# Optimization experiments

Measured on AMD Instinct MI355X. Metric: run time of the kernel, lower is better.

## Reference

```python
import jax, jax.numpy as jnp
import numpy as np


def _cumsum_reset_on_zeros(x):
    # Segmented cumsum along the last axis that resets to 0 at positions where x == 0.
    # Equivalent to the torch trick (inject -diff at zero positions then cumsum):
    # result[i] = cumsum(x)[i] - cumsum(x)[last zero position <= i] (0 if none).
    accum = jnp.cumsum(x, axis=-1)
    pos = jnp.arange(x.shape[-1])
    last_zero = jax.lax.cummax(jnp.where(x == 0, pos, -1), axis=x.ndim - 1)
    baseline = jnp.where(last_zero >= 0, accum[jnp.maximum(last_zero, 0)], jnp.zeros((), accum.dtype))
    return accum - baseline


def _shift_right(x):
    # shift last axis right by one, inserting a leading zero (pad+roll+narrow in torch)
    return jnp.concatenate([jnp.zeros((1,), x.dtype), x[:-1]], axis=-1)


def _adsr(gate, attack, decay, sustain, release):
    one = jnp.float32(1.0)
    ad_axis = _cumsum_reset_on_zeros(gate)          # samples since note-on, 0 while gate off
    attack_mask = (ad_axis <= attack).astype(gate.dtype) * gate
    decay_mask = (ad_axis > attack).astype(gate.dtype) * gate
    release_mask = one - gate
    decay_tc = jnp.exp(-one / decay)                # 1/e**(1/decay)
    release_tc = jnp.exp(-one / release)
    decay_slope = sustain + (one - sustain) * jnp.power(decay_tc, ad_axis - attack)

    # ---- release slope: exp of segmented cumsum of log(release_tc), seeded by decay value at note-off
    ri = decay_slope * jnp.roll(release_mask, -1, axis=-1) * decay_mask  # decay value at last gated sample
    ri = _shift_right(ri)                                                # move seed into first release sample
    ri = jnp.where(ri == 0, one, ri)
    ri = ri * (jnp.cumsum(gate, axis=-1) > 0).astype(gate.dtype)         # zero before the first note
    ri = ri * release_mask * release_tc
    log_rs = jnp.where(ri > 0, jnp.log(jnp.where(ri > 0, ri, one)), 0.0)  # log(0) -> 0, as in torch
    cum_log = _cumsum_reset_on_zeros(log_rs)
    release_slope = jnp.where(cum_log == 0, 0.0, jnp.exp(cum_log))        # 0 -> -inf -> exp -> 0

    # ---- attack slope: ramp from the release level at (re)trigger up to 1
    attack_start = release_slope * jnp.roll(attack_mask, -1, axis=-1) * release_mask
    attack_start = jnp.cumsum(_shift_right(attack_start), axis=-1)
    attack_slope = (one - attack_start) * ad_axis / attack + attack_start

    return attack_slope * attack_mask + decay_slope * decay_mask + release_slope * release_mask


def setup_inputs() -> dict:
    T = 1 << 23  # ~175 s of audio at 48 kHz
    phase = jnp.arange(T) % 48000
    # realistic note pattern: gate high for 24000 samples (0.5 s) per 1 s period,
    # starting with a silent region to exercise the pre-first-note path
    gate = ((phase >= 12000) & (phase < 36000)).astype(jnp.float32)
    return {
        "gate": gate,
        "attack": jnp.float32(480.0),
        "decay": jnp.float32(4800.0),
        "sustain": jnp.float32(0.5),
        "release": jnp.float32(9600.0),
    }


def reference(gate, attack, decay, sustain, release):
    return _adsr(gate, attack, decay, sustain, release)
```

## Files before the change

kernel.cpp:

```cpp
#include <hip/hip_runtime.h>
#include <math.h>

#define SEG_CAP 2048
#define SORT_CAP 8192

struct SegRec { float p0; int type; };

__device__ __forceinline__ float wave_scan_f(float v) {
#pragma unroll
    for (int d = 1; d < 64; d <<= 1) {
        float n = __shfl_up(v, d, 64);
        if ((threadIdx.x & 63) >= d) v += n;
    }
    return v;
}

__global__ void k_collect(const float* __restrict__ g, int T,
                          int* __restrict__ trans, int* __restrict__ counter, int cap) {
    const int tid = threadIdx.x;
    const long nq = (long)T >> 2;
    const long stride = (long)gridDim.x * blockDim.x;
    for (long q = (long)blockIdx.x * blockDim.x + tid; q < nq; q += stride) {
        const long i = q << 2;
        const float4 v = *reinterpret_cast<const float4*>(g + i);
        float prev = __shfl_up(v.w, 1, 64);
        if ((tid & 63) == 0) prev = (i > 0) ? g[i - 1] : v.x;
        int m = 0;
        if (v.x != prev) m |= 1;
        if (v.y != v.x)  m |= 2;
        if (v.z != v.y)  m |= 4;
        if (v.w != v.z)  m |= 8;
        if (m) {
            const int c = __popc(m);
            int base = atomicAdd(counter, c);
            if (m & 1) { if (base < cap) trans[base] = (int)i;     ++base; }
            if (m & 2) { if (base < cap) trans[base] = (int)i + 1; ++base; }
            if (m & 4) { if (base < cap) trans[base] = (int)i + 2; ++base; }
            if (m & 8) { if (base < cap) trans[base] = (int)i + 3; ++base; }
        }
    }
    if (blockIdx.x == 0 && tid == 0) {
        for (long i = nq << 2; i < T; ++i) {
            if (i > 0 && g[i] != g[i - 1]) {
                int base = atomicAdd(counter, 1);
                if (base < cap) trans[base] = (int)i;
            }
        }
    }
}

__global__ void __launch_bounds__(1024) k_segs(
    const float* __restrict__ g,
    const int* __restrict__ trans, const int* __restrict__ counter,
    int* __restrict__ seg_starts, SegRec* __restrict__ recs, int* __restrict__ nseg_p,
    const float* __restrict__ attack_p, const float* __restrict__ decay_p,
    const float* __restrict__ sustain_p, const float* __restrict__ release_p) {
    __shared__ int s_tr[SORT_CAP];
    __shared__ float lds[16];
    const int tid = threadIdx.x;
    const int lane = tid & 63, w = tid >> 6;

    int ntrans = *counter;
    if (ntrans > SORT_CAP) ntrans = SORT_CAP;

    int S = 2;
    while (S < ntrans) S <<= 1;
    for (int i = tid; i < S; i += 1024) s_tr[i] = (i < ntrans) ? trans[i] : 0x7FFFFFFF;
    __syncthreads();
    for (int k = 2; k <= S; k <<= 1) {
        for (int jj = k >> 1; jj > 0; jj >>= 1) {
            for (int idx = tid; idx < S; idx += 1024) {
                const int ixj = idx ^ jj;
                if (ixj > idx) {
                    const int a = s_tr[idx], b = s_tr[ixj];
                    const bool up = ((idx & k) == 0);
                    if ((a > b) == up) { s_tr[idx] = b; s_tr[ixj] = a; }
                }
            }
            __syncthreads();
        }
    }

    const float attack = *attack_p, decay = *decay_p;
    const float sustain = *sustain_p, release = *release_p;
    const float dlog2 = log2f(expf(-1.0f / decay));
    const float rlog2 = log2f(expf(-1.0f / release));
    const bool g0 = (g[0] != 0.0f);
    const int nseg = ntrans + 1;
    if (tid == 0) *nseg_p = nseg;

    float carry = 0.0f;
    for (int basej = 0; basej < nseg; basej += 1024) {
        const int j = basej + tid;
        const bool valid = (j < nseg);
        int start = 0;
        bool gated = false;
        float r = 0.0f;
        if (valid) {
            start = (j == 0) ? 0 : s_tr[j - 1];
            gated = ((j & 1) == 0) ? g0 : !g0;
            if (gated && j >= 2) {
                const int startm1 = s_tr[j - 2];
                const int startm2 = (j == 2) ? 0 : s_tr[j - 3];
                const float lenprev = (float)(startm1 - startm2);
                const float seedp = (lenprev > attack)
                                        ? (sustain + (1.0f - sustain) * exp2f((lenprev - attack) * dlog2))
                                        : 1.0f;
                const float gap = (float)(start - startm1);
                if (1.0f <= attack) r = seedp * exp2f(gap * rlog2);
            }
        }
        float s = wave_scan_f(r);
        if (lane == 63) lds[w] = s;
        __syncthreads();
        if (w == 0) {
            float t = (lane < 16) ? lds[lane] : 0.0f;
#pragma unroll
            for (int d = 1; d < 16; d <<= 1) {
                float nn = __shfl_up(t, d, 64);
                if (lane >= d) t += nn;
            }
            if (lane < 16) lds[lane] = t;
        }
        __syncthreads();
        const float add = (w == 0) ? 0.0f : lds[w - 1];
        const float incl = s + add;
        const float tile_total = lds[15];
        if (valid) {
            seg_starts[j] = start;
            SegRec rec;
            if (gated) {
                rec.type = 1;
                rec.p0 = carry + incl;
            } else if (j == 0) {
                rec.type = 0;
                rec.p0 = 0.0f;
            } else {
                const int sp = (j == 1) ? 0 : s_tr[j - 2];
                const float len = (float)(start - sp);
                rec.type = 2;
                rec.p0 = (len > attack)
                             ? (sustain + (1.0f - sustain) * exp2f((len - attack) * dlog2))
                             : 1.0f;
            }
            recs[j] = rec;
        }
        __syncthreads();
        carry += tile_total;
    }
}

__global__ void k_out(float* __restrict__ out, int T,
                      const int* __restrict__ seg_starts, const SegRec* __restrict__ recs,
                      const int* __restrict__ nseg_p,
                      const float* __restrict__ attack_p, const float* __restrict__ decay_p,
                      const float* __restrict__ sustain_p, const float* __restrict__ release_p) {
    __shared__ int s_start[SEG_CAP];
    __shared__ float s_p0[SEG_CAP];
    __shared__ int s_type[SEG_CAP];
    const int nseg = *nseg_p;
    const bool useLds = (nseg <= SEG_CAP);
    if (useLds) {
        for (int j = threadIdx.x; j < nseg; j += blockDim.x) {
            s_start[j] = seg_starts[j];
            SegRec r = recs[j];
            s_p0[j] = r.p0;
            s_type[j] = r.type;
        }
        __syncthreads();
    }
    const float attack = *attack_p, decay = *decay_p;
    const float sustain = *sustain_p, release = *release_p;
    const float dlog2 = log2f(expf(-1.0f / decay));
    const float rlog2 = log2f(expf(-1.0f / release));
    const float inv_attack = 1.0f / attack;

    const long i0 = ((long)blockIdx.x * blockDim.x + threadIdx.x) * 4;
    if (i0 >= T) return;

    int lo = 0, hi = nseg - 1;
    if (useLds) {
        while (lo < hi) { int mid = (lo + hi + 1) >> 1; if (s_start[mid] <= i0) lo = mid; else hi = mid - 1; }
    } else {
        while (lo < hi) { int mid = (lo + hi + 1) >> 1; if (seg_starts[mid] <= i0) lo = mid; else hi = mid - 1; }
    }
    int j = lo;
    float res[4];
#pragma unroll
    for (int e = 0; e < 4; ++e) {
        const long i = i0 + e;
        if (i < T) {
            if (useLds) { while (j + 1 < nseg && s_start[j + 1] <= i) ++j; }
            else        { while (j + 1 < nseg && seg_starts[j + 1] <= i) ++j; }
            const int   type = useLds ? s_type[j] : recs[j].type;
            const float p0   = useLds ? s_p0[j]   : recs[j].p0;
            const int   st   = useLds ? s_start[j] : seg_starts[j];
            float v;
            if (type == 1) {
                const float ad = (float)(i - st + 1);
                if (ad <= attack) v = (1.0f - p0) * ad * inv_attack + p0;
                else              v = sustain + (1.0f - sustain) * exp2f((ad - attack) * dlog2);
            } else if (type == 2) {
                const float k = (float)(i - st + 1);
                v = p0 * exp2f(k * rlog2);
            } else {
                v = 0.0f;
            }
            res[e] = v;
        } else {
            res[e] = 0.0f;
        }
    }
    if (i0 + 3 < T) {
        *reinterpret_cast<float4*>(out + i0) = make_float4(res[0], res[1], res[2], res[3]);
    } else {
        for (int e = 0; e < 4; ++e)
            if (i0 + e < T) out[i0 + e] = res[e];
    }
}

extern "C" void kernel_launch(void* const* d_in, const int* in_sizes, int n_in,
                              void* d_out, int out_size, void* d_ws, size_t ws_size,
                              hipStream_t stream) {
    const float* gate    = (const float*)d_in[0];
    const float* attack  = (const float*)d_in[1];
    const float* decay   = (const float*)d_in[2];
    const float* sustain = (const float*)d_in[3];
    const float* release = (const float*)d_in[4];
    float* out = (float*)d_out;
    const int T = in_sizes[0];

    char* w = (char*)d_ws;
    int* counter = (int*)w;
    int* nseg_p  = (int*)(w + 8);
    int* trans      = (int*)(w + 256);
    int* seg_starts = trans + SORT_CAP;
    SegRec* recs    = (SegRec*)(seg_starts + SORT_CAP + 2);

    hipMemsetAsync(counter, 0, sizeof(int), stream);

    const int collect_blocks = 2048;
    k_collect<<<collect_blocks, 256, 0, stream>>>(gate, T, trans, counter, SORT_CAP);
    k_segs<<<1, 1024, 0, stream>>>(gate, trans, counter, seg_starts, recs, nseg_p,
                                   attack, decay, sustain, release);
    const int g3 = (int)(((long)T / 4 + 255) / 256);
    k_out<<<g3, 256, 0, stream>>>(out, T, seg_starts, recs, nseg_p,
                                  attack, decay, sustain, release);
}
```

Baseline: 56.50 us.

## Replace atomic transition gather and bitonic sort with per-chunk ordered slots and scan

The transition collector now gives each 4096-sample chunk a fixed slot region. Positions are written in order using a block-level prefix scan over per-thread counts, which replaces the global atomic counter. The single-block segment kernel then compacts these slots with a scan, so the bitonic sort and the memset launch are no longer needed. In exchange, any chunk with more than 16 transitions is silently truncated, and the segment kernel now has to loop over all chunk counts (about 2048) serially in one block.

```diff
diff --git a/kernel.cpp b/kernel.cpp
--- a/kernel.cpp
+++ b/kernel.cpp
@@ -1,11 +1,23 @@
 #include <hip/hip_runtime.h>
 #include <math.h>
 
+#define CHUNK 4096
+#define K1_BLOCK 256
+#define EPT 16
+#define KSLOT 16
+#define SORT_CAP 8192
 #define SEG_CAP 2048
-#define SORT_CAP 8192
 
 struct SegRec { float p0; int type; };
 
+__device__ __forceinline__ int wave_scan_i(int v) {
+#pragma unroll
+    for (int d = 1; d < 64; d <<= 1) {
+        int n = __shfl_up(v, d, 64);
+        if ((threadIdx.x & 63) >= d) v += n;
+    }
+    return v;
+}
 __device__ __forceinline__ float wave_scan_f(float v) {
 #pragma unroll
     for (int d = 1; d < 64; d <<= 1) {
@@ -16,70 +28,103 @@
 }
 
 __global__ void k_collect(const float* __restrict__ g, int T,
-                          int* __restrict__ trans, int* __restrict__ counter, int cap) {
+                          int* __restrict__ counts, int* __restrict__ chunk_tr) {
     const int tid = threadIdx.x;
-    const long nq = (long)T >> 2;
-    const long stride = (long)gridDim.x * blockDim.x;
-    for (long q = (long)blockIdx.x * blockDim.x + tid; q < nq; q += stride) {
-        const long i = q << 2;
-        const float4 v = *reinterpret_cast<const float4*>(g + i);
-        float prev = __shfl_up(v.w, 1, 64);
-        if ((tid & 63) == 0) prev = (i > 0) ? g[i - 1] : v.x;
-        int m = 0;
-        if (v.x != prev) m |= 1;
-        if (v.y != v.x)  m |= 2;
-        if (v.z != v.y)  m |= 4;
-        if (v.w != v.z)  m |= 8;
-        if (m) {
-            const int c = __popc(m);
-            int base = atomicAdd(counter, c);
-            if (m & 1) { if (base < cap) trans[base] = (int)i;     ++base; }
-            if (m & 2) { if (base < cap) trans[base] = (int)i + 1; ++base; }
-            if (m & 4) { if (base < cap) trans[base] = (int)i + 2; ++base; }
-            if (m & 8) { if (base < cap) trans[base] = (int)i + 3; ++base; }
-        }
-    }
-    if (blockIdx.x == 0 && tid == 0) {
-        for (long i = nq << 2; i < T; ++i) {
-            if (i > 0 && g[i] != g[i - 1]) {
-                int base = atomicAdd(counter, 1);
-                if (base < cap) trans[base] = (int)i;
-            }
+    const long base = (long)blockIdx.x * CHUNK + (long)tid * EPT;
+    float vals[EPT];
+    float prevFirst = 0.0f;
+    int n = 0;
+    if (base < T) {
+        const long rem = (long)T - base;
+        n = (int)(rem < EPT ? rem : (long)EPT);
+        prevFirst = (base > 0) ? g[base - 1] : 0.0f;
+        if (n == EPT) {
+#pragma unroll
+            for (int q = 0; q < EPT / 4; ++q) {
+                const float4 v = *reinterpret_cast<const float4*>(g + base + q * 4);
+                vals[q * 4 + 0] = v.x; vals[q * 4 + 1] = v.y;
+                vals[q * 4 + 2] = v.z; vals[q * 4 + 3] = v.w;
+            }
+        } else {
+            for (int e = 0; e < n; ++e) vals[e] = g[base + e];
+        }
+    }
+    int c = 0;
+    {
+        float prev = prevFirst;
+        for (int e = 0; e < n; ++e) {
+            const long i = base + e;
+            if (i > 0 && vals[e] != prev) ++c;
+            prev = vals[e];
+        }
+    }
+    __shared__ int lds[K1_BLOCK / 64];
+    const int lane = tid & 63, w = tid >> 6;
+    const int s = wave_scan_i(c);
+    if (lane == 63) lds[w] = s;
+    __syncthreads();
+    int add = 0;
+#pragma unroll
+    for (int q = 0; q < K1_BLOCK / 64; ++q) add += (q < w) ? lds[q] : 0;
+    int pos = s + add - c;
+    const int total = lds[0] + lds[1] + lds[2] + lds[3];
+    if (tid == 0) counts[blockIdx.x] = (total < KSLOT) ? total : KSLOT;
+    {
+        float prev = prevFirst;
+        for (int e = 0; e < n; ++e) {
+            const long i = base + e;
+            if (i > 0 && vals[e] != prev) {
+                if (pos < KSLOT) chunk_tr[(long)blockIdx.x * KSLOT + pos] = (int)i;
+                ++pos;
+            }
+            prev = vals[e];
         }
     }
 }
 
 __global__ void __launch_bounds__(1024) k_segs(
-    const float* __restrict__ g,
-    const int* __restrict__ trans, const int* __restrict__ counter,
+    const float* __restrict__ g, int nchunk,
+    const int* __restrict__ counts, const int* __restrict__ chunk_tr,
     int* __restrict__ seg_starts, SegRec* __restrict__ recs, int* __restrict__ nseg_p,
     const float* __restrict__ attack_p, const float* __restrict__ decay_p,
     const float* __restrict__ sustain_p, const float* __restrict__ release_p) {
     __shared__ int s_tr[SORT_CAP];
-    __shared__ float lds[16];
+    __shared__ int ldsi[16];
+    __shared__ float ldsf[16];
     const int tid = threadIdx.x;
     const int lane = tid & 63, w = tid >> 6;
 
-    int ntrans = *counter;
-    if (ntrans > SORT_CAP) ntrans = SORT_CAP;
-
-    int S = 2;
-    while (S < ntrans) S <<= 1;
-    for (int i = tid; i < S; i += 1024) s_tr[i] = (i < ntrans) ? trans[i] : 0x7FFFFFFF;
+    int carry = 0;
+    for (int cb = 0; cb < nchunk; cb += 1024) {
+        const int cidx = cb + tid;
+        int cnt = (cidx < nchunk) ? counts[cidx] : 0;
+        if (cnt > KSLOT) cnt = KSLOT;
+        if (cnt < 0) cnt = 0;
+        const int s = wave_scan_i(cnt);
+        if (lane == 63) ldsi[w] = s;
+        __syncthreads();
+        if (w == 0) {
+            int t = (lane < 16) ? ldsi[lane] : 0;
+#pragma unroll
+            for (int d = 1; d < 16; d <<= 1) {
+                const int nn = __shfl_up(t, d, 64);
+                if (lane >= d) t += nn;
+            }
+            if (lane < 16) ldsi[lane] = t;
+        }
+        __syncthreads();
+        const int add = (w == 0) ? 0 : ldsi[w - 1];
+        int off = carry + s + add - cnt;
+        for (int e = 0; e < cnt; ++e) {
+            const int idx = off + e;
+            if (idx < SORT_CAP) s_tr[idx] = chunk_tr[(long)cidx * KSLOT + e];
+        }
+        const int tile_total = ldsi[15];
+        __syncthreads();
+        carry += tile_total;
+    }
+    int ntrans = (carry < SORT_CAP) ? carry : SORT_CAP;
     __syncthreads();
-    for (int k = 2; k <= S; k <<= 1) {
-        for (int jj = k >> 1; jj > 0; jj >>= 1) {
-            for (int idx = tid; idx < S; idx += 1024) {
-                const int ixj = idx ^ jj;
-                if (ixj > idx) {
-                    const int a = s_tr[idx], b = s_tr[ixj];
-                    const bool up = ((idx & k) == 0);
-                    if ((a > b) == up) { s_tr[idx] = b; s_tr[ixj] = a; }
-                }
-            }
-            __syncthreads();
-        }
-    }
 
     const float attack = *attack_p, decay = *decay_p;
     const float sustain = *sustain_p, release = *release_p;
@@ -89,7 +134,7 @@
     const int nseg = ntrans + 1;
     if (tid == 0) *nseg_p = nseg;
 
-    float carry = 0.0f;
+    float fcarry = 0.0f;
     for (int basej = 0; basej < nseg; basej += 1024) {
         const int j = basej + tid;
         const bool valid = (j < nseg);
@@ -111,27 +156,27 @@
             }
         }
         float s = wave_scan_f(r);
-        if (lane == 63) lds[w] = s;
+        if (lane == 63) ldsf[w] = s;
         __syncthreads();
         if (w == 0) {
-            float t = (lane < 16) ? lds[lane] : 0.0f;
+            float t = (lane < 16) ? ldsf[lane] : 0.0f;
 #pragma unroll
             for (int d = 1; d < 16; d <<= 1) {
-                float nn = __shfl_up(t, d, 64);
+                const float nn = __shfl_up(t, d, 64);
                 if (lane >= d) t += nn;
             }
-            if (lane < 16) lds[lane] = t;
-        }
-        __syncthreads();
-        const float add = (w == 0) ? 0.0f : lds[w - 1];
+            if (lane < 16) ldsf[lane] = t;
+        }
+        __syncthreads();
+        const float add = (w == 0) ? 0.0f : ldsf[w - 1];
         const float incl = s + add;
-        const float tile_total = lds[15];
+        const float tile_total = ldsf[15];
         if (valid) {
             seg_starts[j] = start;
             SegRec rec;
             if (gated) {
                 rec.type = 1;
-                rec.p0 = carry + incl;
+                rec.p0 = fcarry + incl;
             } else if (j == 0) {
                 rec.type = 0;
                 rec.p0 = 0.0f;
@@ -146,7 +191,7 @@
             recs[j] = rec;
         }
         __syncthreads();
-        carry += tile_total;
+        fcarry += tile_total;
     }
 }
 
@@ -229,19 +274,18 @@
     const float* release = (const float*)d_in[4];
     float* out = (float*)d_out;
     const int T = in_sizes[0];
+    const int nchunk = (T + CHUNK - 1) / CHUNK;
 
     char* w = (char*)d_ws;
-    int* counter = (int*)w;
-    int* nseg_p  = (int*)(w + 8);
-    int* trans      = (int*)(w + 256);
-    int* seg_starts = trans + SORT_CAP;
+    int* nseg_p     = (int*)(w + 8);
+    int* counts     = (int*)(w + 256);
+    int* chunk_tr   = counts + nchunk;
+    int* seg_starts = chunk_tr + (long)nchunk * KSLOT;
     SegRec* recs    = (SegRec*)(seg_starts + SORT_CAP + 2);
 
-    hipMemsetAsync(counter, 0, sizeof(int), stream);
-
-    const int collect_blocks = 2048;
-    k_collect<<<collect_blocks, 256, 0, stream>>>(gate, T, trans, counter, SORT_CAP);
-    k_segs<<<1, 1024, 0, stream>>>(gate, trans, counter, seg_starts, recs, nseg_p,
+    k_collect<<<nchunk, K1_BLOCK, 0, stream>>>(gate, T, counts, chunk_tr);
+    k_segs<<<1, 1024, 0, stream>>>(gate, nchunk, counts, chunk_tr,
+                                   seg_starts, recs, nseg_p,
                                    attack, decay, sustain, release);
     const int g3 = (int)(((long)T / 4 + 255) / 256);
     k_out<<<g3, 256, 0, stream>>>(out, T, seg_starts, recs, nseg_p,
```

New measurement: 47.14 us. 1.2x faster.
